# Kernel tuning notes

Measured on AMD Instinct MI355X. Metric: run time of the kernel, lower is better.

Reference implementation:

```python
import jax, jax.numpy as jnp
import numpy as np

DIM, HEADS, WH, WW, NPROMPT, NW, BATCH = 384, 12, 7, 7, 5, 64, 32
N = WH * WW + NPROMPT  # 54


def _make_rel_index():
    ch, cw = np.meshgrid(np.arange(WH), np.arange(WW), indexing='ij')
    coords = np.stack([ch, cw]).reshape(2, -1)  # [2, 49]
    rel = coords[:, :, None] - coords[:, None, :]  # [2,49,49]
    rel = rel.transpose(1, 2, 0)
    rel[:, :, 0] += WH - 1
    rel[:, :, 1] += WW - 1
    rel[:, :, 0] *= 2 * WW - 1
    return rel.sum(-1).astype(np.int32)  # [49,49]


def setup_inputs() -> dict:
    key = jax.random.key(0)
    ks = jax.random.split(key, 7)
    B_ = BATCH * NW
    x = jax.random.normal(ks[0], (B_, N, DIM), jnp.float32)
    # 0/-inf style shifted-window mask; random floats exercise the same math
    mask = jnp.where(jax.random.uniform(ks[1], (NW, WH * WW, WH * WW)) > 0.8,
                     jnp.float32(-100.0), jnp.float32(0.0))
    qkv_w = 0.02 * jax.random.normal(ks[2], (3 * DIM, DIM), jnp.float32)
    qkv_b = 0.02 * jax.random.normal(ks[3], (3 * DIM,), jnp.float32)
    proj_w = 0.02 * jax.random.normal(ks[4], (DIM, DIM), jnp.float32)
    proj_b = 0.02 * jax.random.normal(ks[5], (DIM,), jnp.float32)
    rpb_table = 0.02 * jax.random.normal(ks[6], ((2 * WH - 1) * (2 * WW - 1), HEADS), jnp.float32)
    rel_index = jnp.asarray(_make_rel_index())
    return {"x": x, "mask": mask, "qkv_w": qkv_w, "qkv_b": qkv_b,
            "proj_w": proj_w, "proj_b": proj_b, "rpb_table": rpb_table,
            "rel_index": rel_index}


def reference(x, mask, qkv_w, qkv_b, proj_w, proj_b, rpb_table, rel_index):
    B_, n, C = x.shape
    hd = C // HEADS
    scale = hd ** -0.5
    qkv = (x @ qkv_w.T + qkv_b).reshape(B_, n, 3, HEADS, hd)
    qkv = jnp.moveaxis(qkv, 2, 0)  # [3, B_, n, H, hd]
    q, k, v = qkv[0], qkv[1], qkv[2]  # [B_, n, H, hd]
    attn = jnp.einsum('bnhd,bmhd->bhnm', q * scale, k)  # [B_, H, n, n]
    nw2 = WH * WW
    bias = rpb_table[rel_index.reshape(-1)].reshape(nw2, nw2, HEADS)
    bias = jnp.transpose(bias, (2, 0, 1))  # [H, 49, 49]
    bias = jnp.pad(bias, ((0, 0), (NPROMPT, 0), (NPROMPT, 0)))  # [H, n, n]
    attn = attn + bias[None]
    nW = mask.shape[0]
    mask_p = jnp.pad(mask, ((0, 0), (NPROMPT, 0), (NPROMPT, 0)))  # [nW, n, n]
    attn = attn.reshape(B_ // nW, nW, HEADS, n, n) + mask_p[None, :, None]
    attn = jax.nn.softmax(attn.reshape(B_, HEADS, n, n), axis=-1)
    out = jnp.einsum('bhnm,bmhd->bnhd', attn, v).reshape(B_, n, C)
    return out @ proj_w.T + proj_b
```

## Files before the change

kernel.cpp:

```cpp
#include <hip/hip_runtime.h>

#define DIM 384
#define NH 12
#define NT 54
#define NWIN 64
#define MTOT 110592
#define HS ((size_t)MTOT * 32)

typedef __attribute__((ext_vector_type(8))) short short8;
typedef __attribute__((ext_vector_type(4))) float f32x4;

__device__ __forceinline__ unsigned short f2bf(float f) {
  unsigned int u = __float_as_uint(f);
  u += 0x7fffu + ((u >> 16) & 1u);
  return (unsigned short)(u >> 16);
}
__device__ __forceinline__ float bf2f(unsigned short s) {
  return __uint_as_float((unsigned int)s << 16);
}
__device__ __forceinline__ unsigned int cvtpk(float a, float b) {
  unsigned int r;
  asm("v_cvt_pk_bf16_f32 %0, %1, %2" : "=v"(r) : "v"(a), "v"(b));
  return r;
}
__device__ __forceinline__ void gload16(const unsigned short* g,
                                        unsigned short* l) {
  __builtin_amdgcn_global_load_lds(
      (const __attribute__((address_space(1))) void*)g,
      (__attribute__((address_space(3))) void*)l, 16, 0, 0);
}

__global__ __launch_bounds__(256) void convert_x(
    const float* __restrict__ x, unsigned short* __restrict__ xb) {
  const size_t i8 = ((size_t)blockIdx.x * 256 + threadIdx.x) * 8;
  float4 fa = *(const float4*)&x[i8];
  float4 fb = *(const float4*)&x[i8 + 4];
  uint4 u;
  u.x = cvtpk(fa.x, fa.y);
  u.y = cvtpk(fa.z, fa.w);
  u.z = cvtpk(fb.x, fb.y);
  u.w = cvtpk(fb.z, fb.w);
  *(uint4*)&xb[i8] = u;
}

__global__ __launch_bounds__(256) void prep2_kernel(
    const float* __restrict__ qkv_w, const float* __restrict__ proj_w,
    const float* __restrict__ mask, const float* __restrict__ rpb,
    const int* __restrict__ rel,
    unsigned short* __restrict__ Wq, unsigned short* __restrict__ Wp,
    unsigned short* __restrict__ bmt) {
  int idx = blockIdx.x * 256 + threadIdx.x;
  if (idx < 1152 * 384) { Wq[idx] = f2bf(qkv_w[idx]); return; }
  idx -= 1152 * 384;
  if (idx < 384 * 384) { Wp[idx] = f2bf(proj_w[idx]); return; }
  idx -= 384 * 384;
  if (idx < NWIN * NH * 64 * 64) {
    int w = idx / (NH * 4096);
    int rem = idx - w * (NH * 4096);
    int h = rem >> 12, r = (rem >> 6) & 63, c = rem & 63;
    float v;
    if (r >= NT || c >= NT) v = -1e30f;
    else if (r >= 5 && c >= 5)
      v = rpb[rel[(r - 5) * 49 + (c - 5)] * NH + h] +
          mask[w * 2401 + (r - 5) * 49 + (c - 5)];
    else v = 0.0f;
    bmt[w * (NH * 4096) + (h << 12) + (c << 6) + r] = f2bf(v);
  }
}

__global__ __launch_bounds__(256) void qkv_gemm5(
    const unsigned short* __restrict__ xb, const unsigned short* __restrict__ Wq,
    const float* __restrict__ qkv_b,
    unsigned short* __restrict__ Qb, unsigned short* __restrict__ Kb,
    unsigned short* __restrict__ Vb) {
  __shared__ unsigned short As[128][64];
  __shared__ unsigned short Bs[128][64];
  const int s = blockIdx.x;
  const int xcd = s & 7, slot = s >> 3;
  const size_t m0 = (size_t)(xcd * 108 + slot / 9) * 128;
  const int n0 = (slot % 9) * 128;
  const int tid = threadIdx.x;
  const int wv = tid >> 6, ln = tid & 63, g = ln >> 4, lc = ln & 15;
  const int wr = (wv >> 1) * 64, wc = (wv & 1) * 64;
  const int l7 = lc & 7;
  const int lr8 = ln >> 3;
  const int sc8 = (((ln & 7) ^ lr8) & 7) * 8;

  f32x4 acc[4][4];
#pragma unroll
  for (int i = 0; i < 4; ++i)
#pragma unroll
    for (int j = 0; j < 4; ++j) acc[i][j] = (f32x4){0.f, 0.f, 0.f, 0.f};

#pragma unroll
  for (int kc = 0; kc < 6; ++kc) {
    const int k0 = kc * 64;
    if (kc) __syncthreads();
#pragma unroll
    for (int it = 0; it < 4; ++it) {
      const int r0 = wv * 32 + it * 8;
      const int r = r0 + lr8;
      gload16(&xb[(m0 + r) * 384 + k0 + sc8], &As[r0][0]);
      gload16(&Wq[(size_t)(n0 + r) * 384 + k0 + sc8], &Bs[r0][0]);
    }
    __syncthreads();
#pragma unroll
    for (int kk = 0; kk < 2; ++kk) {
      const int cix = (((kk * 4 + g) ^ l7)) * 8;
      short8 af[4], bfv[4];
#pragma unroll
      for (int ms = 0; ms < 4; ++ms)
        af[ms] = *(const short8*)&As[wr + ms * 16 + lc][cix];
#pragma unroll
      for (int ns = 0; ns < 4; ++ns)
        bfv[ns] = *(const short8*)&Bs[wc + ns * 16 + lc][cix];
#pragma unroll
      for (int ms = 0; ms < 4; ++ms)
#pragma unroll
        for (int ns = 0; ns < 4; ++ns)
          acc[ms][ns] = __builtin_amdgcn_mfma_f32_16x16x32_bf16(
              af[ms], bfv[ns], acc[ms][ns], 0, 0, 0);
    }
  }

  const int sel = n0 / 384;
  const float factor = (sel == 0) ? 0.17677669529663687f : 1.0f;
  unsigned short* outp = (sel == 0) ? Qb : (sel == 1 ? Kb : Vb);
#pragma unroll
  for (int ns = 0; ns < 4; ++ns) {
    const int n = n0 + wc + ns * 16 + lc;
    const int rl = n - sel * 384;
    const int h = rl >> 5, d = rl & 31;
    const float bias = qkv_b[n];
#pragma unroll
    for (int ms = 0; ms < 4; ++ms) {
      const size_t mrow = m0 + wr + ms * 16 + g * 4;
      const float v0 = (acc[ms][ns][0] + bias) * factor;
      const float v1 = (acc[ms][ns][1] + bias) * factor;
      const float v2 = (acc[ms][ns][2] + bias) * factor;
      const float v3 = (acc[ms][ns][3] + bias) * factor;
      const unsigned int u01 = cvtpk(v0, v1);
      const unsigned int u23 = cvtpk(v2, v3);
      unsigned short* p = &outp[(size_t)h * HS + mrow * 32 + d];
      p[0]  = (unsigned short)(u01 & 0xffffu);
      p[32] = (unsigned short)(u01 >> 16);
      p[64] = (unsigned short)(u23 & 0xffffu);
      p[96] = (unsigned short)(u23 >> 16);
    }
  }
}

__global__ __launch_bounds__(256) void attn2_kernel(
    unsigned short* __restrict__ Qb, const unsigned short* __restrict__ Kb,
    const unsigned short* __restrict__ Vb, const unsigned short* __restrict__ bmt) {
  __shared__ unsigned short Ps[NT][72];
  __shared__ unsigned short vT[32][72];
  const int s = blockIdx.x;
  const int xcd = s & 7, r3 = s >> 3;
  const int h = r3 % 12;
  const int t2 = r3 / 12;
  const int batch = t2 & 31;
  const int w = xcd * 8 + (t2 >> 5);
  const int b = batch * 64 + w;
  const int tid = threadIdx.x;
  const int wv = tid >> 6, ln = tid & 63, g = ln >> 4, lc = ln & 15;
  const int m0 = wv * 16;
  const size_t base = (size_t)b * NT;
  const int arow = (m0 + lc < NT) ? (m0 + lc) : (NT - 1);
  unsigned short* Qh = Qb + (size_t)h * HS;
  const unsigned short* Kh = Kb + (size_t)h * HS;
  const unsigned short* Vh = Vb + (size_t)h * HS;

  for (int i = tid; i < 320; i += 256) {
    int d = i / 10, m = NT + (i - d * 10);
    vT[d][m] = 0;
  }

  const int vr = tid >> 2, vc = (tid & 3) * 8;
  short8 vv;
  if (tid < 216)
    vv = *(const short8*)&Vh[(base + vr) * 32 + vc];

  short8 a = *(const short8*)&Qh[(base + arow) * 32 + g * 8];
  const unsigned short* bmh = &bmt[(size_t)(w * NH + h) << 12];
  const int row0 = m0 + g * 4;
  f32x4 sac[4];
#pragma unroll
  for (int t = 0; t < 4; ++t) {
    const int col = t * 16 + lc;
    const int kr = (col < NT) ? col : (NT - 1);
    short8 kb = *(const short8*)&Kh[(base + kr) * 32 + g * 8];
    uint2 uu = *(const uint2*)&bmh[(col << 6) + row0];
    f32x4 c0;
    c0[0] = bf2f((unsigned short)(uu.x & 0xffffu));
    c0[1] = bf2f((unsigned short)(uu.x >> 16));
    c0[2] = bf2f((unsigned short)(uu.y & 0xffffu));
    c0[3] = bf2f((unsigned short)(uu.y >> 16));
    sac[t] = __builtin_amdgcn_mfma_f32_16x16x32_bf16(a, kb, c0, 0, 0, 0);
  }
  float rmax[4] = {-3.0e38f, -3.0e38f, -3.0e38f, -3.0e38f};
#pragma unroll
  for (int t = 0; t < 4; ++t)
#pragma unroll
    for (int rr = 0; rr < 4; ++rr) rmax[rr] = fmaxf(rmax[rr], sac[t][rr]);
#pragma unroll
  for (int rr = 0; rr < 4; ++rr)
#pragma unroll
    for (int off = 1; off < 16; off <<= 1)
      rmax[rr] = fmaxf(rmax[rr], __shfl_xor(rmax[rr], off));
  float rsum[4] = {0.f, 0.f, 0.f, 0.f};
#pragma unroll
  for (int t = 0; t < 4; ++t)
#pragma unroll
    for (int rr = 0; rr < 4; ++rr) {
      float p = __expf(sac[t][rr] - rmax[rr]);
      sac[t][rr] = p;
      rsum[rr] += p;
    }
#pragma unroll
  for (int rr = 0; rr < 4; ++rr) {
#pragma unroll
    for (int off = 1; off < 16; off <<= 1)
      rsum[rr] += __shfl_xor(rsum[rr], off);
    rsum[rr] = 1.0f / rsum[rr];
  }
#pragma unroll
  for (int t = 0; t < 4; ++t) {
    const int col = t * 16 + lc;
    const unsigned int u01 = cvtpk(sac[t][0] * rsum[0], sac[t][1] * rsum[1]);
    const unsigned int u23 = cvtpk(sac[t][2] * rsum[2], sac[t][3] * rsum[3]);
    if (row0 < NT)     Ps[row0][col]     = (unsigned short)(u01 & 0xffffu);
    if (row0 + 1 < NT) Ps[row0 + 1][col] = (unsigned short)(u01 >> 16);
    if (row0 + 2 < NT) Ps[row0 + 2][col] = (unsigned short)(u23 & 0xffffu);
    if (row0 + 3 < NT) Ps[row0 + 3][col] = (unsigned short)(u23 >> 16);
  }
  if (tid < 216) {
#pragma unroll
    for (int j = 0; j < 8; ++j) vT[vc + j][vr] = (unsigned short)vv[j];
  }
  __syncthreads();
  f32x4 oac[2];
  oac[0] = (f32x4){0.f, 0.f, 0.f, 0.f};
  oac[1] = (f32x4){0.f, 0.f, 0.f, 0.f};
#pragma unroll
  for (int k2 = 0; k2 < 2; ++k2) {
    short8 pa = *(const short8*)&Ps[arow][k2 * 32 + g * 8];
#pragma unroll
    for (int tn = 0; tn < 2; ++tn) {
      short8 vb = *(const short8*)&vT[tn * 16 + lc][k2 * 32 + g * 8];
      oac[tn] = __builtin_amdgcn_mfma_f32_16x16x32_bf16(pa, vb, oac[tn], 0, 0, 0);
    }
  }
#pragma unroll
  for (int tn = 0; tn < 2; ++tn) {
    const int d = tn * 16 + lc;
    const unsigned int u01 = cvtpk(oac[tn][0], oac[tn][1]);
    const unsigned int u23 = cvtpk(oac[tn][2], oac[tn][3]);
    unsigned short* p = &Qh[(base + row0) * 32 + d];
    if (row0 < NT)     p[0]  = (unsigned short)(u01 & 0xffffu);
    if (row0 + 1 < NT) p[32] = (unsigned short)(u01 >> 16);
    if (row0 + 2 < NT) p[64] = (unsigned short)(u23 & 0xffffu);
    if (row0 + 3 < NT) p[96] = (unsigned short)(u23 >> 16);
  }
}

__global__ __launch_bounds__(256) void proj_hmajor(
    const unsigned short* __restrict__ AO, const unsigned short* __restrict__ Wp,
    const float* __restrict__ proj_b, float* __restrict__ out) {
  __shared__ unsigned short As[128][64];
  __shared__ unsigned short Bs[128][64];
  const int s = blockIdx.x;
  const int xcd = s & 7, slot = s >> 3;
  const size_t m0 = (size_t)(xcd * 108 + slot / 3) * 128;
  const int n0 = (slot % 3) * 128;
  const int tid = threadIdx.x;
  const int wv = tid >> 6, ln = tid & 63, g = ln >> 4, lc = ln & 15;
  const int wr = (wv >> 1) * 64, wc = (wv & 1) * 64;
  const int l7 = lc & 7;
  const int lr8 = ln >> 3;
  const int sc8 = (((ln & 7) ^ lr8) & 7) * 8;

  f32x4 acc[4][4];
#pragma unroll
  for (int i = 0; i < 4; ++i)
#pragma unroll
    for (int j = 0; j < 4; ++j) acc[i][j] = (f32x4){0.f, 0.f, 0.f, 0.f};

#pragma unroll
  for (int kc = 0; kc < 6; ++kc) {
    const int kg = kc * 64 + sc8;
    const int hh = kg >> 5, dd = kg & 31;
    if (kc) __syncthreads();
#pragma unroll
    for (int it = 0; it < 4; ++it) {
      const int r0 = wv * 32 + it * 8;
      const int r = r0 + lr8;
      gload16(&AO[(size_t)hh * HS + (m0 + r) * 32 + dd], &As[r0][0]);
      gload16(&Wp[(size_t)(n0 + r) * 384 + kg], &Bs[r0][0]);
    }
    __syncthreads();
#pragma unroll
    for (int kk = 0; kk < 2; ++kk) {
      const int cix = (((kk * 4 + g) ^ l7)) * 8;
      short8 af[4], bfv[4];
#pragma unroll
      for (int ms = 0; ms < 4; ++ms)
        af[ms] = *(const short8*)&As[wr + ms * 16 + lc][cix];
#pragma unroll
      for (int ns = 0; ns < 4; ++ns)
        bfv[ns] = *(const short8*)&Bs[wc + ns * 16 + lc][cix];
#pragma unroll
      for (int ms = 0; ms < 4; ++ms)
#pragma unroll
        for (int ns = 0; ns < 4; ++ns)
          acc[ms][ns] = __builtin_amdgcn_mfma_f32_16x16x32_bf16(
              af[ms], bfv[ns], acc[ms][ns], 0, 0, 0);
    }
  }

#pragma unroll
  for (int ns = 0; ns < 4; ++ns) {
    const int n = n0 + wc + ns * 16 + lc;
    const float pb = proj_b[n];
#pragma unroll
    for (int ms = 0; ms < 4; ++ms)
#pragma unroll
      for (int rr = 0; rr < 4; ++rr) {
        const size_t m = m0 + wr + ms * 16 + g * 4 + rr;
        out[m * 384 + n] = acc[ms][ns][rr] + pb;
      }
  }
}

__global__ __launch_bounds__(256) void prep_kernel(
    const float* __restrict__ qkv_w, const float* __restrict__ proj_w,
    const float* __restrict__ mask, const float* __restrict__ rpb,
    const int* __restrict__ rel,
    unsigned short* __restrict__ Wq, unsigned short* __restrict__ Wp,
    float* __restrict__ bias_tab, float* __restrict__ maskp) {
  int idx = blockIdx.x * 256 + threadIdx.x;
  if (idx < 1152 * 384) { Wq[idx] = f2bf(qkv_w[idx]); return; }
  idx -= 1152 * 384;
  if (idx < 384 * 384) { Wp[idx] = f2bf(proj_w[idx]); return; }
  idx -= 384 * 384;
  if (idx < NH * 64 * 64) {
    int h = idx >> 12, r = (idx >> 6) & 63, c = idx & 63;
    float v;
    if (r >= NT || c >= NT) v = -1e30f;
    else if (r >= 5 && c >= 5) v = rpb[rel[(r - 5) * 49 + (c - 5)] * NH + h];
    else v = 0.0f;
    bias_tab[idx] = v;
    return;
  }
  idx -= NH * 64 * 64;
  if (idx < NWIN * 64 * 64) {
    int w = idx >> 12, r = (idx >> 6) & 63, c = idx & 63;
    float v = 0.0f;
    if (r >= 5 && r < NT && c >= 5 && c < NT)
      v = mask[w * 2401 + (r - 5) * 49 + (c - 5)];
    maskp[idx] = v;
  }
}

__global__ __launch_bounds__(256) void fused_attn(
    const float* __restrict__ x, const unsigned short* __restrict__ Wq,
    const float* __restrict__ qkv_b, const float* __restrict__ bias_tab,
    const float* __restrict__ maskp, unsigned short* __restrict__ AO) {
  __shared__ unsigned short xs[NT][392];
  __shared__ unsigned short qs[NT][40];
  __shared__ unsigned short ksm[NT][40];
  __shared__ unsigned short vT[32][72];
  __shared__ unsigned short Ps[NT][72];
  const int b = blockIdx.x;
  const int tid = threadIdx.x;
  const int wv = tid >> 6, ln = tid & 63;
  const int g = ln >> 4, lc = ln & 15;
  const int m0 = wv * 16;
  const int wi = b & 63;
  const float scale = 0.17677669529663687f;
  const float* xb = x + (size_t)b * (NT * DIM);
  for (int i = tid; i < NT * DIM / 4; i += 256) {
    float4 v = ((const float4*)xb)[i];
    int e = i * 4, r = e / DIM, c = e - r * DIM;
    unsigned short* p = &xs[r][c];
    p[0] = f2bf(v.x); p[1] = f2bf(v.y); p[2] = f2bf(v.z); p[3] = f2bf(v.w);
  }
  __syncthreads();
  const int arow = (m0 + lc < NT) ? (m0 + lc) : (NT - 1);
  for (int h = 0; h < NH; ++h) {
    f32x4 acc[6];
#pragma unroll
    for (int t = 0; t < 6; ++t) acc[t] = (f32x4){0.f, 0.f, 0.f, 0.f};
#pragma unroll 2
    for (int kk = 0; kk < 12; ++kk) {
      short8 a = *(const short8*)&xs[arow][kk * 32 + g * 8];
#pragma unroll
      for (int t = 0; t < 6; ++t) {
        const int sel = t >> 1;
        const int wrow = sel * 384 + h * 32 + (t & 1) * 16 + lc;
        short8 bfr = *(const short8*)&Wq[wrow * 384 + kk * 32 + g * 8];
        acc[t] = __builtin_amdgcn_mfma_f32_16x16x32_bf16(a, bfr, acc[t], 0, 0, 0);
      }
    }
#pragma unroll
    for (int t = 0; t < 6; ++t) {
      const int sel = t >> 1;
      const int d = (t & 1) * 16 + lc;
      const float bias = qkv_b[sel * 384 + h * 32 + d];
#pragma unroll
      for (int r = 0; r < 4; ++r) {
        const int m = m0 + g * 4 + r;
        float v = acc[t][r] + bias;
        if (sel == 2) vT[d][m] = f2bf(v);
        else if (m < NT) {
          if (sel == 0) qs[m][d] = f2bf(v * scale);
          else ksm[m][d] = f2bf(v);
        }
      }
    }
    __syncthreads();
    f32x4 sac[4];
    {
      short8 a = *(const short8*)&qs[arow][g * 8];
#pragma unroll
      for (int t = 0; t < 4; ++t) {
        const int kr = (t * 16 + lc < NT) ? (t * 16 + lc) : (NT - 1);
        short8 bfr = *(const short8*)&ksm[kr][g * 8];
        sac[t] = __builtin_amdgcn_mfma_f32_16x16x32_bf16(
            a, bfr, (f32x4){0.f, 0.f, 0.f, 0.f}, 0, 0, 0);
      }
    }
    const float* bt = bias_tab + h * 4096;
    const float* mp = maskp + wi * 4096;
    float sv[4][4];
    float rmax[4];
#pragma unroll
    for (int r = 0; r < 4; ++r) rmax[r] = -3.0e38f;
#pragma unroll
    for (int t = 0; t < 4; ++t) {
      const int col = t * 16 + lc;
#pragma unroll
      for (int r = 0; r < 4; ++r) {
        const int row = m0 + g * 4 + r;
        float s = sac[t][r] + bt[row * 64 + col] + mp[row * 64 + col];
        sv[t][r] = s;
        rmax[r] = fmaxf(rmax[r], s);
      }
    }
#pragma unroll
    for (int r = 0; r < 4; ++r)
#pragma unroll
      for (int off = 1; off < 16; off <<= 1)
        rmax[r] = fmaxf(rmax[r], __shfl_xor(rmax[r], off));
    float rsum[4] = {0.f, 0.f, 0.f, 0.f};
#pragma unroll
    for (int t = 0; t < 4; ++t)
#pragma unroll
      for (int r = 0; r < 4; ++r) {
        float p = __expf(sv[t][r] - rmax[r]);
        sv[t][r] = p;
        rsum[r] += p;
      }
#pragma unroll
    for (int r = 0; r < 4; ++r) {
#pragma unroll
      for (int off = 1; off < 16; off <<= 1)
        rsum[r] += __shfl_xor(rsum[r], off);
      rsum[r] = 1.0f / rsum[r];
    }
#pragma unroll
    for (int t = 0; t < 4; ++t) {
      const int col = t * 16 + lc;
#pragma unroll
      for (int r = 0; r < 4; ++r) {
        const int row = m0 + g * 4 + r;
        if (row < NT) Ps[row][col] = f2bf(sv[t][r] * rsum[r]);
      }
    }
    __syncthreads();
    f32x4 oac[2];
    oac[0] = (f32x4){0.f, 0.f, 0.f, 0.f};
    oac[1] = (f32x4){0.f, 0.f, 0.f, 0.f};
#pragma unroll
    for (int k2 = 0; k2 < 2; ++k2) {
      short8 a = *(const short8*)&Ps[arow][k2 * 32 + g * 8];
#pragma unroll
      for (int tn = 0; tn < 2; ++tn) {
        short8 bfr = *(const short8*)&vT[tn * 16 + lc][k2 * 32 + g * 8];
        oac[tn] = __builtin_amdgcn_mfma_f32_16x16x32_bf16(a, bfr, oac[tn], 0, 0, 0);
      }
    }
    unsigned short* aob = AO + (size_t)b * (NT * DIM) + h * 32;
#pragma unroll
    for (int tn = 0; tn < 2; ++tn) {
      const int d = tn * 16 + lc;
#pragma unroll
      for (int r = 0; r < 4; ++r) {
        const int m = m0 + g * 4 + r;
        if (m < NT) aob[m * DIM + d] = f2bf(oac[tn][r]);
      }
    }
    __syncthreads();
  }
}

__global__ __launch_bounds__(256) void proj_kernel(
    const unsigned short* __restrict__ AO, const unsigned short* __restrict__ Wp,
    const float* __restrict__ proj_b, float* __restrict__ out, int lda) {
  __shared__ unsigned short As[128][72];
  __shared__ unsigned short Bs[128][72];
  const int s = blockIdx.x;
  const int xcd = s & 7, slot = s >> 3;
  const size_t m0 = (size_t)(xcd * 108 + slot / 3) * 128;
  const int n0 = (slot % 3) * 128;
  const int tid = threadIdx.x;
  const int wv = tid >> 6, ln = tid & 63, g = ln >> 4, lc = ln & 15;
  const int wr = (wv >> 1) * 64, wc = (wv & 1) * 64;
  f32x4 acc[4][4];
#pragma unroll
  for (int i = 0; i < 4; ++i)
#pragma unroll
    for (int j = 0; j < 4; ++j) acc[i][j] = (f32x4){0.f, 0.f, 0.f, 0.f};

  const int srow = tid >> 3, l8 = tid & 7;
  for (int kc = 0; kc < 6; ++kc) {
    const int k0 = kc * 64;
#pragma unroll
    for (int it = 0; it < 4; ++it) {
      const int r = srow + it * 32;
      *(short8*)&As[r][l8 * 8] =
          *(const short8*)&AO[(m0 + r) * (size_t)lda + k0 + l8 * 8];
      *(short8*)&Bs[r][l8 * 8] =
          *(const short8*)&Wp[(size_t)(n0 + r) * 384 + k0 + l8 * 8];
    }
    __syncthreads();
#pragma unroll
    for (int kk = 0; kk < 2; ++kk) {
      short8 af[4], bfr[4];
#pragma unroll
      for (int ms = 0; ms < 4; ++ms)
        af[ms] = *(const short8*)&As[wr + ms * 16 + lc][kk * 32 + g * 8];
#pragma unroll
      for (int ns = 0; ns < 4; ++ns)
        bfr[ns] = *(const short8*)&Bs[wc + ns * 16 + lc][kk * 32 + g * 8];
#pragma unroll
      for (int ms = 0; ms < 4; ++ms)
#pragma unroll
        for (int ns = 0; ns < 4; ++ns)
          acc[ms][ns] = __builtin_amdgcn_mfma_f32_16x16x32_bf16(
              af[ms], bfr[ns], acc[ms][ns], 0, 0, 0);
    }
    __syncthreads();
  }
#pragma unroll
  for (int ns = 0; ns < 4; ++ns) {
    const int n = n0 + wc + ns * 16 + lc;
    const float pb = proj_b[n];
#pragma unroll
    for (int ms = 0; ms < 4; ++ms)
#pragma unroll
      for (int rr = 0; rr < 4; ++rr) {
        const size_t m = m0 + wr + ms * 16 + g * 4 + rr;
        out[m * 384 + n] = acc[ms][ns][rr] + pb;
      }
  }
}

extern "C" void kernel_launch(void* const* d_in, const int* in_sizes, int n_in,
                              void* d_out, int out_size, void* d_ws, size_t ws_size,
                              hipStream_t stream) {
  const float* x      = (const float*)d_in[0];
  const float* mask   = (const float*)d_in[1];
  const float* qkv_w  = (const float*)d_in[2];
  const float* qkv_b  = (const float*)d_in[3];
  const float* proj_w = (const float*)d_in[4];
  const float* proj_b = (const float*)d_in[5];
  const float* rpb    = (const float*)d_in[6];
  const int*   rel    = (const int*)d_in[7];
  float* out = (float*)d_out;

  const size_t QKV_ELEMS = (size_t)3 * NH * HS;
  const size_t WQ_ELEMS = 1152 * 384, WP_ELEMS = 384 * 384;
  const size_t BMT_ELEMS = (size_t)NWIN * NH * 4096;
  const size_t need = (QKV_ELEMS + WQ_ELEMS + WP_ELEMS + BMT_ELEMS) * 2;

  if (ws_size >= need) {
    unsigned short* Qb  = (unsigned short*)d_ws;
    unsigned short* Kb  = Qb + NH * HS;
    unsigned short* Vb  = Kb + NH * HS;
    unsigned short* Wq  = Vb + NH * HS;
    unsigned short* Wp  = Wq + WQ_ELEMS;
    unsigned short* bmt = Wp + WP_ELEMS;
    unsigned short* xb = (unsigned short*)d_out;

    convert_x<<<20736, 256, 0, stream>>>(x, xb);
    prep2_kernel<<<14592, 256, 0, stream>>>(qkv_w, proj_w, mask, rpb, rel,
                                            Wq, Wp, bmt);
    qkv_gemm5<<<7776, 256, 0, stream>>>(xb, Wq, qkv_b, Qb, Kb, Vb);
    attn2_kernel<<<24576, 256, 0, stream>>>(Qb, Kb, Vb, bmt);
    proj_hmajor<<<2592, 256, 0, stream>>>(Qb, Wp, proj_b, out);
  } else {
    unsigned short* Wq = (unsigned short*)d_ws;
    unsigned short* Wp = Wq + 442368;
    float* bias_tab = (float*)(Wp + 147456);
    float* maskp = bias_tab + 12 * 64 * 64;
    unsigned short* AO = (unsigned short*)(maskp + 64 * 64 * 64);
    prep_kernel<<<3520, 256, 0, stream>>>(qkv_w, proj_w, mask, rpb, rel,
                                          Wq, Wp, bias_tab, maskp);
    fused_attn<<<2048, 256, 0, stream>>>(x, Wq, qkv_b, bias_tab, maskp, AO);
    proj_kernel<<<2592, 256, 0, stream>>>(AO, Wp, proj_b, out, 384);
  }
}
```

Measured before the change: 419.0 us.

## Batch K/bias loads in attention and use padded LDS staging in projection GEMM

In the attention kernel, all four K-fragment and bias loads are issued before any MFMA, so their memory latency overlaps instead of being serialised per tile. The projection GEMM drops its direct global-to-LDS loads and XOR swizzle. It now copies tiles through registers into LDS padded to 72 columns to avoid bank conflicts, with a trailing barrier and the k-loop no longer force-unrolled. The register round trip adds VGPR pressure and instructions, and the padded layout may read less efficiently than the swizzle.

Result: no change. 415.7 us (-0.8%).

```diff
diff --git a/kernel.cpp b/kernel.cpp
--- a/kernel.cpp
+++ b/kernel.cpp
@@ -184,19 +184,25 @@
   short8 a = *(const short8*)&Qh[(base + arow) * 32 + g * 8];
   const unsigned short* bmh = &bmt[(size_t)(w * NH + h) << 12];
   const int row0 = m0 + g * 4;
-  f32x4 sac[4];
+  short8 kb[4];
+  uint2 uu[4];
 #pragma unroll
   for (int t = 0; t < 4; ++t) {
     const int col = t * 16 + lc;
     const int kr = (col < NT) ? col : (NT - 1);
-    short8 kb = *(const short8*)&Kh[(base + kr) * 32 + g * 8];
-    uint2 uu = *(const uint2*)&bmh[(col << 6) + row0];
+    kb[t] = *(const short8*)&Kh[(base + kr) * 32 + g * 8];
+    uu[t] = *(const uint2*)&bmh[(col << 6) + row0];
+  }
+
+  f32x4 sac[4];
+#pragma unroll
+  for (int t = 0; t < 4; ++t) {
     f32x4 c0;
-    c0[0] = bf2f((unsigned short)(uu.x & 0xffffu));
-    c0[1] = bf2f((unsigned short)(uu.x >> 16));
-    c0[2] = bf2f((unsigned short)(uu.y & 0xffffu));
-    c0[3] = bf2f((unsigned short)(uu.y >> 16));
-    sac[t] = __builtin_amdgcn_mfma_f32_16x16x32_bf16(a, kb, c0, 0, 0, 0);
+    c0[0] = bf2f((unsigned short)(uu[t].x & 0xffffu));
+    c0[1] = bf2f((unsigned short)(uu[t].x >> 16));
+    c0[2] = bf2f((unsigned short)(uu[t].y & 0xffffu));
+    c0[3] = bf2f((unsigned short)(uu[t].y >> 16));
+    sac[t] = __builtin_amdgcn_mfma_f32_16x16x32_bf16(a, kb[t], c0, 0, 0, 0);
   }
   float rmax[4] = {-3.0e38f, -3.0e38f, -3.0e38f, -3.0e38f};
 #pragma unroll
@@ -267,8 +273,8 @@
 __global__ __launch_bounds__(256) void proj_hmajor(
     const unsigned short* __restrict__ AO, const unsigned short* __restrict__ Wp,
     const float* __restrict__ proj_b, float* __restrict__ out) {
-  __shared__ unsigned short As[128][64];
-  __shared__ unsigned short Bs[128][64];
+  __shared__ unsigned short As[128][72];
+  __shared__ unsigned short Bs[128][72];
   const int s = blockIdx.x;
   const int xcd = s & 7, slot = s >> 3;
   const size_t m0 = (size_t)(xcd * 108 + slot / 3) * 128;
@@ -276,39 +282,35 @@
   const int tid = threadIdx.x;
   const int wv = tid >> 6, ln = tid & 63, g = ln >> 4, lc = ln & 15;
   const int wr = (wv >> 1) * 64, wc = (wv & 1) * 64;
-  const int l7 = lc & 7;
-  const int lr8 = ln >> 3;
-  const int sc8 = (((ln & 7) ^ lr8) & 7) * 8;
-
   f32x4 acc[4][4];
 #pragma unroll
   for (int i = 0; i < 4; ++i)
 #pragma unroll
     for (int j = 0; j < 4; ++j) acc[i][j] = (f32x4){0.f, 0.f, 0.f, 0.f};
 
-#pragma unroll
+  const int srow = tid >> 3, l8 = tid & 7;
   for (int kc = 0; kc < 6; ++kc) {
-    const int kg = kc * 64 + sc8;
+    const int k0 = kc * 64;
+    const int kg = k0 + l8 * 8;
     const int hh = kg >> 5, dd = kg & 31;
-    if (kc) __syncthreads();
 #pragma unroll
     for (int it = 0; it < 4; ++it) {
-      const int r0 = wv * 32 + it * 8;
-      const int r = r0 + lr8;
-      gload16(&AO[(size_t)hh * HS + (m0 + r) * 32 + dd], &As[r0][0]);
-      gload16(&Wp[(size_t)(n0 + r) * 384 + kg], &Bs[r0][0]);
+      const int r = srow + it * 32;
+      *(short8*)&As[r][l8 * 8] =
+          *(const short8*)&AO[(size_t)hh * HS + (m0 + r) * 32 + dd];
+      *(short8*)&Bs[r][l8 * 8] =
+          *(const short8*)&Wp[(size_t)(n0 + r) * 384 + kg];
     }
     __syncthreads();
 #pragma unroll
     for (int kk = 0; kk < 2; ++kk) {
-      const int cix = (((kk * 4 + g) ^ l7)) * 8;
       short8 af[4], bfv[4];
 #pragma unroll
       for (int ms = 0; ms < 4; ++ms)
-        af[ms] = *(const short8*)&As[wr + ms * 16 + lc][cix];
+        af[ms] = *(const short8*)&As[wr + ms * 16 + lc][kk * 32 + g * 8];
 #pragma unroll
       for (int ns = 0; ns < 4; ++ns)
-        bfv[ns] = *(const short8*)&Bs[wc + ns * 16 + lc][cix];
+        bfv[ns] = *(const short8*)&Bs[wc + ns * 16 + lc][kk * 32 + g * 8];
 #pragma unroll
       for (int ms = 0; ms < 4; ++ms)
 #pragma unroll
@@ -316,8 +318,8 @@
           acc[ms][ns] = __builtin_amdgcn_mfma_f32_16x16x32_bf16(
               af[ms], bfv[ns], acc[ms][ns], 0, 0, 0);
     }
-  }
-
+    __syncthreads();
+  }
 #pragma unroll
   for (int ns = 0; ns < 4; ++ns) {
     const int n = n0 + wc + ns * 16 + lc;
@@ -442,9 +444,9 @@
 #pragma unroll
       for (int r = 0; r < 4; ++r) {
         const int row = m0 + g * 4 + r;
-        float s = sac[t][r] + bt[row * 64 + col] + mp[row * 64 + col];
-        sv[t][r] = s;
-        rmax[r] = fmaxf(rmax[r], s);
+        float s2 = sac[t][r] + bt[row * 64 + col] + mp[row * 64 + col];
+        sv[t][r] = s2;
+        rmax[r] = fmaxf(rmax[r], s2);
       }
     }
 #pragma unroll
```
